# Kernel optimization log

Hardware: AMD Instinct MI355X
Metric: run time of the kernel (lower is better)

Reference implementation:

```python
import jax, jax.numpy as jnp
import numpy as np

N_NODES = 100000
N_EDGES = 1600000
IN_CH = 64
HID = 64
OUT_CH = 32


def _init_lin(key, fan_in, fan_out):
    # uniform(-1/sqrt(fan_in), 1/sqrt(fan_in)) like torch Linear
    b = 1.0 / np.sqrt(fan_in)
    return jax.random.uniform(key, (fan_in, fan_out), jnp.float32, -b, b)


def setup_inputs() -> dict:
    key = jax.random.key(0)
    ks = jax.random.split(key, 16)
    x = jax.random.normal(ks[0], (N_NODES, IN_CH), jnp.float32)
    edge_index = jax.random.randint(ks[1], (2, N_EDGES), 0, N_NODES, jnp.int64)
    params = {}
    dims = [(IN_CH, HID), (HID, HID), (HID, HID)]
    for i, (fi, fo) in enumerate(dims, start=1):
        params[f"Wl{i}"] = _init_lin(ks[3 * i], fi, fo)       # applied to aggregated neighbors
        params[f"Wr{i}"] = _init_lin(ks[3 * i + 1], fi, fo)   # applied to root features
        params[f"b{i}"] = jnp.zeros((fo,), jnp.float32)
    params["Wlin"] = _init_lin(ks[12], HID, OUT_CH)
    params["blin"] = jnp.zeros((OUT_CH,), jnp.float32)
    return {"x": x, "edge_index": edge_index, **params}


def _mean_aggregate(x, src, dst, n_nodes):
    # mean of source-node features over incoming edges per destination node
    msg_sum = jax.ops.segment_sum(x[src], dst, num_segments=n_nodes)
    deg = jax.ops.segment_sum(jnp.ones((src.shape[0], 1), x.dtype), dst, num_segments=n_nodes)
    return msg_sum / jnp.maximum(deg, 1.0)


def _sage_conv(x, src, dst, Wl, Wr, b):
    # PyG SAGEConv (mean aggr): out = lin_l(mean_j x_j) + lin_r(x_i)
    agg = _mean_aggregate(x, src, dst, x.shape[0])
    return agg @ Wl + b + x @ Wr


def reference(x, edge_index, Wl1, Wr1, b1, Wl2, Wr2, b2, Wl3, Wr3, b3, Wlin, blin):
    src, dst = edge_index[0], edge_index[1]
    h = jax.nn.relu(_sage_conv(x, src, dst, Wl1, Wr1, b1))
    h = jax.nn.relu(_sage_conv(h, src, dst, Wl2, Wr2, b2))
    h = jax.nn.relu(_sage_conv(h, src, dst, Wl3, Wr3, b3))
    return h @ Wlin + blin
```

## Files before the change

### kernel.cpp

```cpp
#include <hip/hip_runtime.h>
#include <hip/hip_bf16.h>

#define N_NODES 100000
#define N_EDGES 1600000
#define HID 64
#define OUT_CH 32

#define NB 196
#define P 1024
#define EPP ((N_EDGES + P - 1) / P)
#define BKCAP 10240
#define MP 72

typedef unsigned short ushort_t;
typedef short bf16x8 __attribute__((ext_vector_type(8)));
typedef float f32x4 __attribute__((ext_vector_type(4)));

__device__ __forceinline__ ushort_t f2b(float f) {
    union { float f; unsigned u; } un; un.f = f;
    unsigned r = un.u + 0x7FFF + ((un.u >> 16) & 1);
    return (ushort_t)(r >> 16);
}
__device__ __forceinline__ float b2f(ushort_t u) {
    union { unsigned u; float f; } un; un.u = ((unsigned)u) << 16;
    return un.f;
}
__device__ __forceinline__ float blo(unsigned u) {
    union { unsigned u; float f; } un; un.u = u << 16; return un.f;
}
__device__ __forceinline__ float bhi(unsigned u) {
    union { unsigned u; float f; } un; un.u = u & 0xFFFF0000u; return un.f;
}

__device__ __forceinline__ int get_dst(const int* __restrict__ ei, int is64, int e) {
    return is64 ? ((const int2*)ei)[N_EDGES + e].x : ei[N_EDGES + e];
}
__device__ __forceinline__ int get_src(const int* __restrict__ ei, int is64, int e) {
    return is64 ? ((const int2*)ei)[e].x : ei[e];
}

__device__ __forceinline__ void detect_is64(const int* __restrict__ ei,
                                            int* __restrict__ sflag, int tid) {
    if (tid < 64) {
        int v = ei[2 * tid + 1];
        unsigned long long ball = __ballot(v == 0);
        if (tid == 0) *sflag = (ball == ~0ull) ? 1 : 0;
    }
}

#define CONV_BLOCKS ((N_NODES * HID / 4) / 256)
__global__ void __launch_bounds__(256) convhist_kernel(
        const float* __restrict__ x, ushort_t* __restrict__ xb,
        const int* __restrict__ ei, int* __restrict__ histG,
        const float* __restrict__ W0, const float* __restrict__ W1,
        const float* __restrict__ W2, const float* __restrict__ W3,
        const float* __restrict__ W4, const float* __restrict__ W5,
        ushort_t* __restrict__ wpk) {
    int bid = blockIdx.x;
    if (bid >= CONV_BLOCKS) {
        const float* Ws[6] = {W0, W1, W2, W3, W4, W5};
        int w = bid - CONV_BLOCKS;
        const float* W = Ws[w];
        ushort_t* d = wpk + w * 4096;
        for (int idx = threadIdx.x; idx < 4096; idx += 256) {
            int j = idx & 7;
            int ln = (idx >> 3) & 63;
            int t = idx >> 9;
            int ks = t & 1, nt = t >> 1;
            int k = ks * 32 + (ln >> 4) * 8 + j;
            int n = nt * 16 + (ln & 15);
            d[idx] = f2b(W[k * HID + n]);
        }
        return;
    }
    int i = bid * 256 + threadIdx.x;
    if (i < N_NODES * HID / 4) {
        float4 v = ((const float4*)x)[i];
        ushort4 o;
        o.x = f2b(v.x); o.y = f2b(v.y); o.z = f2b(v.z); o.w = f2b(v.w);
        ((ushort4*)xb)[i] = o;
    }
    if (bid >= P) return;
    __shared__ int sflag;
    __shared__ int lh[NB];
    int tid = threadIdx.x;
    detect_is64(ei, &sflag, tid);
    for (int k = tid; k < NB; k += 256) lh[k] = 0;
    __syncthreads();
    int is64 = sflag;
    int e0 = bid * EPP;
    int e1 = min(e0 + EPP, N_EDGES);
    for (int e = e0 + tid; e < e1; e += 256) {
        int d = get_dst(ei, is64, e);
        atomicAdd(&lh[d >> 9], 1);
    }
    __syncthreads();
    for (int k = tid; k < NB; k += 256) histG[k * P + bid] = lh[k];
}

__global__ void __launch_bounds__(256) scan_kernel(int* __restrict__ histG,
                                                   int* __restrict__ btot) {
    __shared__ int ps[256];
    int b = blockIdx.x;
    int tid = threadIdx.x;
    int base4 = b * P + 4 * tid;
    int v0 = histG[base4], v1 = histG[base4 + 1], v2 = histG[base4 + 2], v3 = histG[base4 + 3];
    int pv = v0 + v1 + v2 + v3;
    ps[tid] = pv;
    __syncthreads();
    for (int d = 1; d < 256; d <<= 1) {
        int t = (tid >= d) ? ps[tid - d] : 0;
        __syncthreads();
        ps[tid] += t;
        __syncthreads();
    }
    int e = ps[tid] - pv;
    histG[base4] = e; e += v0;
    histG[base4 + 1] = e; e += v1;
    histG[base4 + 2] = e; e += v2;
    histG[base4 + 3] = e;
    if (tid == 255) btot[b] = ps[255];
}

__global__ void __launch_bounds__(256) place_kernel(
        const int* __restrict__ ei, const int* __restrict__ histG,
        const int* __restrict__ btot, int* __restrict__ bkt) {
    __shared__ int lcur[NB];
    __shared__ int ss[256];
    __shared__ int sflag;
    int tid = threadIdx.x;
    detect_is64(ei, &sflag, tid);
    int v = (tid < NB) ? btot[tid] : 0;
    ss[tid] = v;
    __syncthreads();
    for (int d = 1; d < 256; d <<= 1) {
        int t = (tid >= d) ? ss[tid - d] : 0;
        __syncthreads();
        ss[tid] += t;
        __syncthreads();
    }
    if (tid < NB) lcur[tid] = (ss[tid] - v) + histG[tid * P + blockIdx.x];
    __syncthreads();
    int is64 = sflag;
    int e0 = blockIdx.x * EPP;
    int e1 = min(e0 + EPP, N_EDGES);
    for (int e = e0 + tid; e < e1; e += 256) {
        int s = get_src(ei, is64, e);
        int d = get_dst(ei, is64, e);
        int val = ((d & 511) << 17) | s;
        int p = atomicAdd(&lcur[d >> 9], 1);
        bkt[p] = val;
    }
}

__global__ void __launch_bounds__(256) bucket_fill_kernel(
        const int* __restrict__ btot, const int* __restrict__ bkt,
        int* __restrict__ csr, unsigned int* __restrict__ offpk) {
    __shared__ int lcnt[512];
    __shared__ int loff[512];
    __shared__ int lcur[512];
    __shared__ int ps[256];
    __shared__ int scsr[BKCAP];
    __shared__ int sbase;
    int b = blockIdx.x;
    int tid = threadIdx.x;
    int m = btot[b];
    int vb = (tid < NB) ? btot[tid] : 0;
    ps[tid] = vb;
    __syncthreads();
    for (int d = 1; d < 256; d <<= 1) {
        int t = (tid >= d) ? ps[tid - d] : 0;
        __syncthreads();
        ps[tid] += t;
        __syncthreads();
    }
    if (tid == b) sbase = ps[tid] - vb;
    __syncthreads();
    int base = sbase;
    int n0 = b << 9;
    int nn = min(512, N_NODES - n0);

    lcnt[tid] = 0;
    lcnt[tid + 256] = 0;
    __syncthreads();
    for (int i = tid; i < m; i += 256) atomicAdd(&lcnt[bkt[base + i] >> 17], 1);
    __syncthreads();
    int a0 = lcnt[2 * tid], a1 = lcnt[2 * tid + 1];
    int pv = a0 + a1;
    ps[tid] = pv;
    __syncthreads();
    for (int d = 1; d < 256; d <<= 1) {
        int t = (tid >= d) ? ps[tid - d] : 0;
        __syncthreads();
        ps[tid] += t;
        __syncthreads();
    }
    int excl = ps[tid] - pv;
    loff[2 * tid] = excl;
    loff[2 * tid + 1] = excl + a0;
    lcur[2 * tid] = excl;
    lcur[2 * tid + 1] = excl + a0;
    __syncthreads();
    bool fit = (m <= BKCAP);
    for (int i = tid; i < m; i += 256) {
        int val = bkt[base + i];
        int dl = val >> 17;
        int p = atomicAdd(&lcur[dl], 1);
        if (fit) scsr[p] = val & 0x1FFFF;
        else csr[base + p] = val & 0x1FFFF;
    }
    __syncthreads();
    if (fit)
        for (int i = tid; i < m; i += 256) csr[base + i] = scsr[i];
    for (int i = tid; i < nn; i += 256)
        offpk[n0 + i] = (unsigned int)((base + loff[i]) | (lcnt[i] << 21));
}

__global__ void __launch_bounds__(256) gather_kernel(
        const ushort_t* __restrict__ hb, const unsigned int* __restrict__ offpk,
        const int* __restrict__ csr, ushort_t* __restrict__ aggb) {
    int node = blockIdx.x * 4 + (threadIdx.x >> 6);
    if (node >= N_NODES) return;
    int o = threadIdx.x & 63;
    int q4 = o >> 4;
    int l = o & 15;
    unsigned int v = offpk[node];
    int off0 = (int)(v & 0x1FFFFFu);
    int cnt = (int)(v >> 21);
    float a0 = 0.f, a1 = 0.f, a2 = 0.f, a3 = 0.f;
    int base = off0;
    int rem = cnt;
    while (rem > 0) {
        int take = min(rem, 64);
        int idxv = (o < take) ? csr[base + o] : 0;
        int j = 0;
        for (; j + 16 <= take; j += 16) {
            int i0 = __shfl(idxv, j + q4);
            int i1 = __shfl(idxv, j + 4 + q4);
            int i2 = __shfl(idxv, j + 8 + q4);
            int i3 = __shfl(idxv, j + 12 + q4);
            int2 u0 = ((const int2*)(hb + (size_t)i0 * HID))[l];
            int2 u1 = ((const int2*)(hb + (size_t)i1 * HID))[l];
            int2 u2 = ((const int2*)(hb + (size_t)i2 * HID))[l];
            int2 u3 = ((const int2*)(hb + (size_t)i3 * HID))[l];
            a0 += (blo(u0.x) + blo(u1.x)) + (blo(u2.x) + blo(u3.x));
            a1 += (bhi(u0.x) + bhi(u1.x)) + (bhi(u2.x) + bhi(u3.x));
            a2 += (blo(u0.y) + blo(u1.y)) + (blo(u2.y) + blo(u3.y));
            a3 += (bhi(u0.y) + bhi(u1.y)) + (bhi(u2.y) + bhi(u3.y));
        }
        for (; j < take; j += 4) {
            int e = j + q4;
            bool valid = (e < take);
            int idx = __shfl(idxv, valid ? e : 0);
            if (valid) {
                int2 u = ((const int2*)(hb + (size_t)idx * HID))[l];
                a0 += blo(u.x); a1 += bhi(u.x);
                a2 += blo(u.y); a3 += bhi(u.y);
            }
        }
        base += take;
        rem -= take;
    }
    a0 += __shfl_xor(a0, 16); a0 += __shfl_xor(a0, 32);
    a1 += __shfl_xor(a1, 16); a1 += __shfl_xor(a1, 32);
    a2 += __shfl_xor(a2, 16); a2 += __shfl_xor(a2, 32);
    a3 += __shfl_xor(a3, 16); a3 += __shfl_xor(a3, 32);
    if (o < 16) {
        float inv = 1.f / fmaxf((float)cnt, 1.f);
        ushort4 w;
        w.x = f2b(a0 * inv); w.y = f2b(a1 * inv);
        w.z = f2b(a2 * inv); w.w = f2b(a3 * inv);
        *(ushort4*)(aggb + (size_t)node * HID + l * 4) = w;
    }
}

template <bool FUSE_HEAD>
__global__ void __launch_bounds__(256) layer_mfma(
        const ushort_t* __restrict__ aggb, const ushort_t* __restrict__ rootb,
        const ushort_t* __restrict__ wpk, const float* __restrict__ bias,
        ushort_t* __restrict__ outb,
        const float* __restrict__ Wlin, const float* __restrict__ blin,
        float* __restrict__ out) {
    __shared__ __align__(16) ushort_t sWlF[4096];
    __shared__ __align__(16) ushort_t sWrF[4096];
    __shared__ __align__(16) ushort_t sA[64 * MP];
    __shared__ __align__(16) ushort_t sH[64 * MP];
    __shared__ float sbias[HID];
    __shared__ float sWo[FUSE_HEAD ? HID * OUT_CH : 1];
    __shared__ float sbo[FUSE_HEAD ? OUT_CH : 1];
    int tid = threadIdx.x;
    {
        const int4* w4 = (const int4*)wpk;
        int4* sl4 = (int4*)sWlF;
        int4* sr4 = (int4*)sWrF;
#pragma unroll
        for (int p = 0; p < 2; ++p) {
            int i = tid + 256 * p;
            sl4[i] = w4[i];
            sr4[i] = w4[512 + i];
        }
    }
    if (tid < HID) sbias[tid] = bias[tid];
    size_t tbase = (size_t)blockIdx.x * 64 * HID;
    {
        const int4* ga = (const int4*)(aggb + tbase);
        const int4* gh = (const int4*)(rootb + tbase);
#pragma unroll
        for (int p = 0; p < 2; ++p) {
            int q = tid + 256 * p;
            int r = q >> 3, u = q & 7;
            *(int4*)(sA + r * MP + u * 8) = ga[q];
            *(int4*)(sH + r * MP + u * 8) = gh[q];
        }
    }
    __syncthreads();

    int wave = tid >> 6, lane = tid & 63;
    int quad = lane >> 4, col = lane & 15;
    int arow = wave * 16 + col;
    bf16x8 aA0 = *(const bf16x8*)(sA + arow * MP + quad * 8);
    bf16x8 aA1 = *(const bf16x8*)(sA + arow * MP + 32 + quad * 8);
    bf16x8 aH0 = *(const bf16x8*)(sH + arow * MP + quad * 8);
    bf16x8 aH1 = *(const bf16x8*)(sH + arow * MP + 32 + quad * 8);
    int node0 = blockIdx.x * 64;
    ushort_t hv[4][4];
#pragma unroll
    for (int nt = 0; nt < 4; ++nt) {
        f32x4 acc = {0.f, 0.f, 0.f, 0.f};
        const bf16x8* bl = (const bf16x8*)(sWlF + nt * 1024);
        const bf16x8* br = (const bf16x8*)(sWrF + nt * 1024);
        acc = __builtin_amdgcn_mfma_f32_16x16x32_bf16(aA0, bl[lane], acc, 0, 0, 0);
        acc = __builtin_amdgcn_mfma_f32_16x16x32_bf16(aA1, bl[64 + lane], acc, 0, 0, 0);
        acc = __builtin_amdgcn_mfma_f32_16x16x32_bf16(aH0, br[lane], acc, 0, 0, 0);
        acc = __builtin_amdgcn_mfma_f32_16x16x32_bf16(aH1, br[64 + lane], acc, 0, 0, 0);
        float bv = sbias[nt * 16 + col];
#pragma unroll
        for (int r = 0; r < 4; ++r) {
            ushort_t hb16 = f2b(fmaxf(acc[r] + bv, 0.f));
            if constexpr (FUSE_HEAD) {
                hv[nt][r] = hb16;
            } else {
                int n = node0 + wave * 16 + quad * 4 + r;
                if (n < N_NODES)
                    outb[(size_t)n * HID + nt * 16 + col] = hb16;
            }
        }
    }

    if constexpr (FUSE_HEAD) {
        __syncthreads();
#pragma unroll
        for (int nt = 0; nt < 4; ++nt)
#pragma unroll
            for (int r = 0; r < 4; ++r)
                sA[(wave * 16 + quad * 4 + r) * MP + nt * 16 + col] = hv[nt][r];
        {
            const int4* W4 = (const int4*)Wlin;
            int4* sW4 = (int4*)sWo;
#pragma unroll
            for (int p = 0; p < 2; ++p) sW4[tid + 256 * p] = W4[tid + 256 * p];
            if (tid < OUT_CH) sbo[tid] = blin[tid];
        }
        __syncthreads();

        int c0 = (tid & 7) << 2;
        int n0 = (tid >> 3) << 1;
        float acc2[2][4];
#pragma unroll
        for (int i = 0; i < 2; ++i)
#pragma unroll
            for (int j = 0; j < 4; ++j) acc2[i][j] = sbo[c0 + j];

#pragma unroll 4
        for (int kk = 0; kk < 32; ++kk) {
            float4 w0 = *(const float4*)&sWo[(2 * kk) * OUT_CH + c0];
            float4 w1 = *(const float4*)&sWo[(2 * kk + 1) * OUT_CH + c0];
            const float* w0p = (const float*)&w0;
            const float* w1p = (const float*)&w1;
#pragma unroll
            for (int i = 0; i < 2; ++i) {
                unsigned uh = *(const unsigned*)(sA + (n0 + i) * MP + 2 * kk);
                float h0 = blo(uh), h1 = bhi(uh);
#pragma unroll
                for (int j = 0; j < 4; ++j) acc2[i][j] += h0 * w0p[j] + h1 * w1p[j];
            }
        }

#pragma unroll
        for (int i = 0; i < 2; ++i) {
            int n = node0 + n0 + i;
            if (n < N_NODES) {
                float4 o4;
                o4.x = acc2[i][0]; o4.y = acc2[i][1];
                o4.z = acc2[i][2]; o4.w = acc2[i][3];
                *(float4*)(out + (size_t)n * OUT_CH + c0) = o4;
            }
        }
    }
}

extern "C" void kernel_launch(void* const* d_in, const int* in_sizes, int n_in,
                              void* d_out, int out_size, void* d_ws, size_t ws_size,
                              hipStream_t stream) {
    const float* x    = (const float*)d_in[0];
    const int*   ei   = (const int*)d_in[1];
    const float* Wl1  = (const float*)d_in[2];
    const float* Wr1  = (const float*)d_in[3];
    const float* b1   = (const float*)d_in[4];
    const float* Wl2  = (const float*)d_in[5];
    const float* Wr2  = (const float*)d_in[6];
    const float* b2   = (const float*)d_in[7];
    const float* Wl3  = (const float*)d_in[8];
    const float* Wr3  = (const float*)d_in[9];
    const float* b3   = (const float*)d_in[10];
    const float* Wlin = (const float*)d_in[11];
    const float* blin = (const float*)d_in[12];
    float* out = (float*)d_out;

    int* ip              = (int*)d_ws;
    unsigned int* offpk  = (unsigned int*)ip;
    int* btot            = (int*)(offpk + 100096);
    int* histG           = btot + 256;
    int* csr             = histG + NB * P;
    ushort_t* aggb       = (ushort_t*)(csr + N_EDGES);
    ushort_t* featb      = aggb + 6408192;
    ushort_t* wpk        = featb + 6408192;
    int* bkt             = (int*)aggb;

    const int GATHER_BLOCKS = (N_NODES + 3) / 4;
    const int TILE_BLOCKS   = (N_NODES + 63) / 64;

    convhist_kernel<<<CONV_BLOCKS + 6, 256, 0, stream>>>(
        x, featb, ei, histG, Wl1, Wr1, Wl2, Wr2, Wl3, Wr3, wpk);
    scan_kernel<<<NB, 256, 0, stream>>>(histG, btot);
    place_kernel<<<P, 256, 0, stream>>>(ei, histG, btot, bkt);
    bucket_fill_kernel<<<NB, 256, 0, stream>>>(btot, bkt, csr, offpk);

    gather_kernel<<<GATHER_BLOCKS, 256, 0, stream>>>(featb, offpk, csr, aggb);
    layer_mfma<false><<<TILE_BLOCKS, 256, 0, stream>>>(
        aggb, featb, wpk, b1, featb, nullptr, nullptr, nullptr);

    gather_kernel<<<GATHER_BLOCKS, 256, 0, stream>>>(featb, offpk, csr, aggb);
    layer_mfma<false><<<TILE_BLOCKS, 256, 0, stream>>>(
        aggb, featb, wpk + 8192, b2, featb, nullptr, nullptr, nullptr);

    gather_kernel<<<GATHER_BLOCKS, 256, 0, stream>>>(featb, offpk, csr, aggb);
    layer_mfma<true><<<TILE_BLOCKS, 256, 0, stream>>>(
        aggb, featb, wpk + 16384, b3, nullptr, Wlin, blin, out);
}
```

Baseline: 295.7 us.

## Remap gather to 8 lanes per node with 16B loads and 16-edge batches

The neighbor-mean gather now gives each node 8 lanes instead of a full 64-lane wavefront, so one wavefront handles 8 nodes. Each lane loads 16 bytes (8 bf16) per neighbor row instead of 8 bytes. It issues 16 independent row loads per batch before accumulating. This is meant to cut lane idling on low-degree nodes and the cross-lane reduction, and to put more memory requests in flight. In exchange it uses more registers for the 16 buffered int4 loads, and lanes in a wavefront diverge when node degrees differ. The grid drops its bounds check and relies on N_NODES being divisible by 32.

```diff
diff --git a/kernel.cpp b/kernel.cpp
--- a/kernel.cpp
+++ b/kernel.cpp
@@ -219,59 +219,44 @@
 __global__ void __launch_bounds__(256) gather_kernel(
         const ushort_t* __restrict__ hb, const unsigned int* __restrict__ offpk,
         const int* __restrict__ csr, ushort_t* __restrict__ aggb) {
-    int node = blockIdx.x * 4 + (threadIdx.x >> 6);
-    if (node >= N_NODES) return;
-    int o = threadIdx.x & 63;
-    int q4 = o >> 4;
-    int l = o & 15;
+    int tid = threadIdx.x;
+    int wv = tid >> 6, ln = tid & 63;
+    int g = ln >> 3;
+    int l = ln & 7;
+    int node = blockIdx.x * 32 + wv * 8 + g;
     unsigned int v = offpk[node];
-    int off0 = (int)(v & 0x1FFFFFu);
+    int off = (int)(v & 0x1FFFFFu);
     int cnt = (int)(v >> 21);
     float a0 = 0.f, a1 = 0.f, a2 = 0.f, a3 = 0.f;
-    int base = off0;
-    int rem = cnt;
-    while (rem > 0) {
-        int take = min(rem, 64);
-        int idxv = (o < take) ? csr[base + o] : 0;
-        int j = 0;
-        for (; j + 16 <= take; j += 16) {
-            int i0 = __shfl(idxv, j + q4);
-            int i1 = __shfl(idxv, j + 4 + q4);
-            int i2 = __shfl(idxv, j + 8 + q4);
-            int i3 = __shfl(idxv, j + 12 + q4);
-            int2 u0 = ((const int2*)(hb + (size_t)i0 * HID))[l];
-            int2 u1 = ((const int2*)(hb + (size_t)i1 * HID))[l];
-            int2 u2 = ((const int2*)(hb + (size_t)i2 * HID))[l];
-            int2 u3 = ((const int2*)(hb + (size_t)i3 * HID))[l];
-            a0 += (blo(u0.x) + blo(u1.x)) + (blo(u2.x) + blo(u3.x));
-            a1 += (bhi(u0.x) + bhi(u1.x)) + (bhi(u2.x) + bhi(u3.x));
-            a2 += (blo(u0.y) + blo(u1.y)) + (blo(u2.y) + blo(u3.y));
-            a3 += (bhi(u0.y) + bhi(u1.y)) + (bhi(u2.y) + bhi(u3.y));
-        }
-        for (; j < take; j += 4) {
-            int e = j + q4;
-            bool valid = (e < take);
-            int idx = __shfl(idxv, valid ? e : 0);
-            if (valid) {
-                int2 u = ((const int2*)(hb + (size_t)idx * HID))[l];
-                a0 += blo(u.x); a1 += bhi(u.x);
-                a2 += blo(u.y); a3 += bhi(u.y);
-            }
-        }
-        base += take;
-        rem -= take;
-    }
-    a0 += __shfl_xor(a0, 16); a0 += __shfl_xor(a0, 32);
-    a1 += __shfl_xor(a1, 16); a1 += __shfl_xor(a1, 32);
-    a2 += __shfl_xor(a2, 16); a2 += __shfl_xor(a2, 32);
-    a3 += __shfl_xor(a3, 16); a3 += __shfl_xor(a3, 32);
-    if (o < 16) {
-        float inv = 1.f / fmaxf((float)cnt, 1.f);
-        ushort4 w;
-        w.x = f2b(a0 * inv); w.y = f2b(a1 * inv);
-        w.z = f2b(a2 * inv); w.w = f2b(a3 * inv);
-        *(ushort4*)(aggb + (size_t)node * HID + l * 4) = w;
-    }
+    float a4 = 0.f, a5 = 0.f, a6 = 0.f, a7 = 0.f;
+    int gbase = g << 3;
+    for (int b = 0; b < cnt; b += 16) {
+        int rem = cnt - b;
+        int e0 = (l < rem) ? csr[off + b + l] : 0;
+        int e1 = (l + 8 < rem) ? csr[off + b + 8 + l] : 0;
+        int4 u[16];
+#pragma unroll
+        for (int j = 0; j < 8; ++j)
+            u[j] = ((const int4*)(hb + (size_t)__shfl(e0, gbase + j) * HID))[l];
+#pragma unroll
+        for (int j = 0; j < 8; ++j)
+            u[8 + j] = ((const int4*)(hb + (size_t)__shfl(e1, gbase + j) * HID))[l];
+#pragma unroll
+        for (int j = 0; j < 16; ++j) {
+            if (j >= rem) { u[j].x = 0; u[j].y = 0; u[j].z = 0; u[j].w = 0; }
+            a0 += blo(u[j].x); a1 += bhi(u[j].x);
+            a2 += blo(u[j].y); a3 += bhi(u[j].y);
+            a4 += blo(u[j].z); a5 += bhi(u[j].z);
+            a6 += blo(u[j].w); a7 += bhi(u[j].w);
+        }
+    }
+    float inv = 1.f / fmaxf((float)cnt, 1.f);
+    int4 w;
+    w.x = (int)((unsigned)f2b(a0 * inv) | ((unsigned)f2b(a1 * inv) << 16));
+    w.y = (int)((unsigned)f2b(a2 * inv) | ((unsigned)f2b(a3 * inv) << 16));
+    w.z = (int)((unsigned)f2b(a4 * inv) | ((unsigned)f2b(a5 * inv) << 16));
+    w.w = (int)((unsigned)f2b(a6 * inv) | ((unsigned)f2b(a7 * inv) << 16));
+    *(int4*)(aggb + (size_t)node * HID + l * 8) = w;
 }
 
 template <bool FUSE_HEAD>
@@ -427,7 +412,7 @@
     ushort_t* wpk        = featb + 6408192;
     int* bkt             = (int*)aggb;
 
-    const int GATHER_BLOCKS = (N_NODES + 3) / 4;
+    const int GATHER_BLOCKS = N_NODES / 32;
     const int TILE_BLOCKS   = (N_NODES + 63) / 64;
 
     convhist_kernel<<<CONV_BLOCKS + 6, 256, 0, stream>>>(
```

Result: faster. 260.0 us (-12.1%).
